# Kernel optimization log

Hardware: AMD Instinct MI355X
Metric: run time of the kernel (lower is better)

Reference implementation:

```python
import jax, jax.numpy as jnp
import numpy as np

B, S, P, I, H, NF, O = 128, 48, 60, 512, 512, 4, 2  # batch, seq_len, pad_size, input_size, hidden, n_filters, output
INITRANGE = 0.1


def setup_inputs() -> dict:
    key = jax.random.key(0)
    ks = jax.random.split(key, 16)
    u = lambda k, shape: jax.random.uniform(k, shape, jnp.float32, -INITRANGE, INITRANGE)
    return {
        "inputs": jax.random.normal(ks[0], (B, S, P, I), jnp.float32),
        # conv: Conv1d(1,1,kernel=input_size,stride=2) == dot product with a length-I vector + scalar bias
        "conv_w": u(ks[1], (I,)),
        "conv_b": u(ks[2], (1,)),
        # bidirectional single-layer GRU params (PyTorch layout: [3H, in], gate order r,z,n)
        "wih_f": u(ks[3], (3 * H, I)), "whh_f": u(ks[4], (3 * H, H)),
        "bih_f": u(ks[5], (3 * H,)), "bhh_f": u(ks[6], (3 * H,)),
        "wih_b": u(ks[7], (3 * H, I)), "whh_b": u(ks[8], (3 * H, H)),
        "bih_b": u(ks[9], (3 * H,)), "bhh_b": u(ks[10], (3 * H,)),
        # conv2: Conv1d(1,n_filters,kernel=hidden*2) == n_filters dot products over the state vector
        "conv2_w": u(ks[11], (NF, 2 * H)),
        "conv2_b": u(ks[12], (NF,)),
        "lin_w": u(ks[13], (O, NF * 2 * H)),
        "lin_b": u(ks[14], (O,)),
        "batch_size": B,
    }


def _gru_dir(x, wih, whh, bih, bhh, reverse):
    # x: [B,S,I]; PyTorch GRU cell math, gate order (r, z, n)
    xp = jnp.einsum("bsi,gi->bsg", x, wih) + bih  # [B,S,3H], input proj hoisted out of scan

    def step(h, xt):
        hp = h @ whh.T + bhh
        xr, xz, xn = jnp.split(xt, 3, axis=-1)
        hr, hz, hn = jnp.split(hp, 3, axis=-1)
        r = jax.nn.sigmoid(xr + hr)
        z = jax.nn.sigmoid(xz + hz)
        n = jnp.tanh(xn + r * hn)
        h_new = (1.0 - z) * n + z * h
        return h_new, h_new

    h0 = jnp.zeros((x.shape[0], whh.shape[1]), x.dtype)
    _, hs = jax.lax.scan(step, h0, jnp.swapaxes(xp, 0, 1), reverse=reverse)
    return jnp.swapaxes(hs, 0, 1)  # [B,S,H], time-major order preserved


def reference(inputs, conv_w, conv_b, wih_f, whh_f, bih_f, bhh_f,
              wih_b, whh_b, bih_b, bhh_b, conv2_w, conv2_b, lin_w, lin_b, batch_size):
    # --- convolutional_layer: per-(visit,code) scalar score, hardtanh(0,1), weighted sum over codes ---
    alpha = jnp.clip(jnp.einsum("bspi,i->bsp", inputs, conv_w) + conv_b[0], 0.0, 1.0)  # [B,S,P]
    emb = jnp.einsum("bsp,bspi->bsi", alpha, inputs)  # [B,S,I]
    # dropout is identity in eval mode
    # --- bidirectional GRU ---
    hf = _gru_dir(emb, wih_f, whh_f, bih_f, bhh_f, reverse=False)
    hb = _gru_dir(emb, wih_b, whh_b, bih_b, bhh_b, reverse=True)
    states = jnp.concatenate([hf, hb], axis=-1)  # [B,S,2H]
    # --- add_beta_attention: n_filters scores per step, softmax over seq, weighted sum of states ---
    logits = jnp.einsum("bsh,fh->bfs", states, conv2_w) + conv2_b[None, :, None]  # [B,F,S]
    beta = jax.nn.softmax(logits, axis=-1)
    context = jnp.einsum("bfs,bsh->bfh", beta, states).reshape(batch_size, -1)  # [B, F*2H]
    out = jax.nn.softmax(context @ lin_w.T + lin_b, axis=-1)  # [B,O]
    return out, alpha, beta
```

## Files before the change

kernel.cpp:

```cpp
#include <hip/hip_runtime.h>

#define B_ 128
#define S_ 48
#define P_ 60
#define I_ 512
#define H_ 512
#define NF_ 4
#define O_ 2

typedef __bf16 bf16x8 __attribute__((ext_vector_type(8)));
typedef float f32x4 __attribute__((ext_vector_type(4)));
typedef unsigned long long u64;

__global__ __launch_bounds__(512, 2) void k_fused(
    const float* __restrict__ inputs, const float* __restrict__ conv_w,
    const float* __restrict__ conv_b,
    const float* __restrict__ whh_f, const float* __restrict__ whh_b,
    const float* __restrict__ wih_f, const float* __restrict__ wih_b,
    const float* __restrict__ bhh_f, const float* __restrict__ bhh_b,
    const float* __restrict__ bih_f, const float* __restrict__ bih_b,
    float* __restrict__ alpha_out,
    unsigned* __restrict__ emb32,
    u64* __restrict__ hbf,
    float* __restrict__ hs,
    unsigned* __restrict__ bar,
    unsigned* __restrict__ percol)
{
  __shared__ __bf16 Ahh[48 * 512];
  __shared__ __bf16 Aih[48 * 512];
  __shared__ float part2[8][512];

  int bid = blockIdx.x;

  if (bid < 128) {
    int dir = bid >> 6;
    int j0  = (bid & 31) * 16;
    int m0  = ((bid >> 5) & 1) * 64;
    int myi = bid & 31;
    int grp = bid >> 5;
    const float* Whh_d = dir ? whh_b : whh_f;
    const float* Wih_d = dir ? wih_b : wih_f;

    for (int it = threadIdx.x; it < 48 * 64; it += 512) {
      int r = it >> 6, c8 = it & 63;
      int grow = (r >> 4) * H_ + j0 + (r & 15);
      int dst = r * 512 + ((c8 ^ (r & 7)) * 8);
      const float* sh = Whh_d + (size_t)grow * I_ + c8 * 8;
      const float* si = Wih_d + (size_t)grow * I_ + c8 * 8;
      float4 a = *(const float4*)(sh), b = *(const float4*)(sh + 4);
      float4 c = *(const float4*)(si), d = *(const float4*)(si + 4);
      bf16x8 oh, oi;
      oh[0]=(__bf16)a.x; oh[1]=(__bf16)a.y; oh[2]=(__bf16)a.z; oh[3]=(__bf16)a.w;
      oh[4]=(__bf16)b.x; oh[5]=(__bf16)b.y; oh[6]=(__bf16)b.z; oh[7]=(__bf16)b.w;
      oi[0]=(__bf16)c.x; oi[1]=(__bf16)c.y; oi[2]=(__bf16)c.z; oi[3]=(__bf16)c.w;
      oi[4]=(__bf16)d.x; oi[5]=(__bf16)d.y; oi[6]=(__bf16)d.z; oi[7]=(__bf16)d.w;
      *(bf16x8*)(Ahh + dst) = oh;
      *(bf16x8*)(Aih + dst) = oi;
    }
    __syncthreads();

    if (threadIdx.x < 256) {
      int wave = threadIdx.x >> 6, lane = threadIdx.x & 63;
      int col = lane & 15, hi = lane >> 4;
      int b = m0 + wave * 16 + col;
      int j = j0 + hi * 4;
      const float* bhh = dir ? bhh_b : bhh_f;
      const float* bih = dir ? bih_b : bih_f;
      float4 bhr = *(const float4*)(bhh + j);
      float4 bhz = *(const float4*)(bhh + H_ + j);
      float4 bhn = *(const float4*)(bhh + 2 * H_ + j);
      float4 bxr = *(const float4*)(bih + j);
      float4 bxz = *(const float4*)(bih + H_ + j);
      float4 bxn = *(const float4*)(bih + 2 * H_ + j);
      float bhhA[3][4] = {{bhr.x,bhr.y,bhr.z,bhr.w},{bhz.x,bhz.y,bhz.z,bhz.w},{bhn.x,bhn.y,bhn.z,bhn.w}};
      float bihA[3][4] = {{bxr.x,bxr.y,bxr.z,bxr.w},{bxz.x,bxz.y,bxz.z,bxz.w},{bxn.x,bxn.y,bxn.z,bxn.w}};
      int rb0 = (0 * 16 + col) * 512, rb1 = (1 * 16 + col) * 512, rb2 = (2 * 16 + col) * 512;
      int csw = col & 7;
      const u64* embB64 = (const u64*)emb32 + (size_t)b * S_ * 128;

      const size_t STEPBUF = (size_t)2 * B_ * (H_ / 4);
      size_t hoff = ((size_t)dir * B_ + b) * (H_ / 4);
      const u64* hd64 = (const u64*)(percol + 48);

      float hprev[4] = {0.f, 0.f, 0.f, 0.f};
      int esent = 0;

      for (int step = 0; step < S_; ++step) {
        int t = dir ? (S_ - 1 - step) : step;

        if (!esent) {
          u64 hd = __hip_atomic_load(hd64, __ATOMIC_RELAXED, __HIP_MEMORY_SCOPE_AGENT);
          if (hd == 0x0000000100000001ull) esent = 1;
          else while (__hip_atomic_load(percol + t, __ATOMIC_RELAXED,
                                        __HIP_MEMORY_SCOPE_AGENT) < 64u) {}
        }

        const u64* erow64 = embB64 + (size_t)t * 128;
        u64 ebu[32];
        #pragma unroll
        for (int kk = 0; kk < 16; ++kk) {
          ebu[2 * kk]     = __hip_atomic_load(erow64 + kk * 8 + hi * 2,
                                              __ATOMIC_RELAXED, __HIP_MEMORY_SCOPE_AGENT);
          ebu[2 * kk + 1] = __hip_atomic_load(erow64 + kk * 8 + hi * 2 + 1,
                                              __ATOMIC_RELAXED, __HIP_MEMORY_SCOPE_AGENT);
        }

        if (step != 0) {
          if (threadIdx.x < 32) {
            const unsigned* pf = bar + (((unsigned)step * 4 + grp) * 32 + threadIdx.x) * 16;
            while (__hip_atomic_load(pf, __ATOMIC_RELAXED, __HIP_MEMORY_SCOPE_AGENT) == 0u) {}
          }
          __syncthreads();
        }

        const u64* hin = hbf + (size_t)step * STEPBUF + hoff;
        u64 hb[32];
        #pragma unroll
        for (int kk = 0; kk < 16; ++kk) {
          hb[2 * kk]     = __hip_atomic_load(hin + kk * 8 + hi * 2, __ATOMIC_RELAXED,
                                             __HIP_MEMORY_SCOPE_AGENT);
          hb[2 * kk + 1] = __hip_atomic_load(hin + kk * 8 + hi * 2 + 1, __ATOMIC_RELAXED,
                                             __HIP_MEMORY_SCOPE_AGENT);
        }

        f32x4 ah0 = {0,0,0,0}, ah1 = {0,0,0,0}, ah2 = {0,0,0,0};
        f32x4 ax0 = {0,0,0,0}, ax1 = {0,0,0,0}, ax2 = {0,0,0,0};
        #pragma unroll
        for (int kk = 0; kk < 16; ++kk) {
          union { u64 u[2]; bf16x8 v; } bu, eu;
          bu.u[0] = hb[2 * kk];
          bu.u[1] = hb[2 * kk + 1];
          eu.u[0] = ebu[2 * kk];
          eu.u[1] = ebu[2 * kk + 1];
          int go = ((kk * 4 + hi) ^ csw) * 8;
          bf16x8 a0 = *(const bf16x8*)(Ahh + rb0 + go);
          bf16x8 a1 = *(const bf16x8*)(Ahh + rb1 + go);
          bf16x8 a2 = *(const bf16x8*)(Ahh + rb2 + go);
          bf16x8 w0 = *(const bf16x8*)(Aih + rb0 + go);
          bf16x8 w1 = *(const bf16x8*)(Aih + rb1 + go);
          bf16x8 w2 = *(const bf16x8*)(Aih + rb2 + go);
          ah0 = __builtin_amdgcn_mfma_f32_16x16x32_bf16(a0, bu.v, ah0, 0, 0, 0);
          ax0 = __builtin_amdgcn_mfma_f32_16x16x32_bf16(w0, eu.v, ax0, 0, 0, 0);
          ah1 = __builtin_amdgcn_mfma_f32_16x16x32_bf16(a1, bu.v, ah1, 0, 0, 0);
          ax1 = __builtin_amdgcn_mfma_f32_16x16x32_bf16(w1, eu.v, ax1, 0, 0, 0);
          ah2 = __builtin_amdgcn_mfma_f32_16x16x32_bf16(a2, bu.v, ah2, 0, 0, 0);
          ax2 = __builtin_amdgcn_mfma_f32_16x16x32_bf16(w2, eu.v, ax2, 0, 0, 0);
        }

        union { u64 u; __bf16 h[4]; } pk;
        #pragma unroll
        for (int r = 0; r < 4; r++) {
          float hr = ah0[r] + bhhA[0][r];
          float hz = ah1[r] + bhhA[1][r];
          float hn = ah2[r] + bhhA[2][r];
          float xr = ax0[r] + bihA[0][r];
          float xz = ax1[r] + bihA[1][r];
          float xn = ax2[r] + bihA[2][r];
          float rg = 1.f / (1.f + __expf(-(xr + hr)));
          float zg = 1.f / (1.f + __expf(-(xz + hz)));
          float ng = tanhf(xn + rg * hn);
          float hnew = (1.f - zg) * ng + zg * hprev[r];
          hprev[r] = hnew;
          pk.h[r] = (__bf16)hnew;
        }

        if (step != S_ - 1) {
          u64* hout = hbf + (size_t)(step + 1) * STEPBUF + hoff;
          __hip_atomic_store(hout + (j0 >> 2) + hi, pk.u, __ATOMIC_RELAXED,
                             __HIP_MEMORY_SCOPE_AGENT);
          __syncthreads();
          if (threadIdx.x == 0)
            __hip_atomic_store(bar + (((unsigned)(step + 1) * 4 + grp) * 32 + myi) * 16,
                               1u, __ATOMIC_RELAXED, __HIP_MEMORY_SCOPE_AGENT);
        }

        float4 hv = {hprev[0], hprev[1], hprev[2], hprev[3]};
        *(float4*)(hs + ((size_t)b * S_ + t) * (2 * H_) + dir * H_ + j) = hv;
      }
    } else {
      for (int step = 0; step < S_; ++step) {
        if (step != 0) __syncthreads();
        if (step != S_ - 1) __syncthreads();
      }
    }
  } else {
    int bid2 = bid - 128;
    int half = bid2 >> 6;
    int blk  = bid2 & 63;
    int bA   = blk * 2;
    int wv   = threadIdx.x >> 6, lane = threadIdx.x & 63;
    int batch = bA + (wv >> 2);
    int wsub  = wv & 3;

    float w[8];
    {
      const float4* c4 = (const float4*)(conv_w + lane * 8);
      float4 a = c4[0], bq = c4[1];
      w[0]=a.x; w[1]=a.y; w[2]=a.z; w[3]=a.w; w[4]=bq.x; w[5]=bq.y; w[6]=bq.z; w[7]=bq.w;
    }
    float cb0 = conv_b[0];

    for (int c = 0; c < 24; ++c) {
      int s = half ? (47 - c) : c;
      const float* xb = inputs + ((size_t)batch * S_ + s) * (P_ * I_);

      float acc[8] = {0,0,0,0,0,0,0,0};
      for (int g = 0; g < 3; ++g) {
        int pbase = wsub + g * 20;
        float xv[5][8];
        float d[5];
        #pragma unroll
        for (int u = 0; u < 5; ++u) {
          const float4* xr = (const float4*)(xb + (size_t)(pbase + 4 * u) * I_ + lane * 8);
          float4 a = xr[0], bq = xr[1];
          xv[u][0]=a.x; xv[u][1]=a.y; xv[u][2]=a.z; xv[u][3]=a.w;
          xv[u][4]=bq.x; xv[u][5]=bq.y; xv[u][6]=bq.z; xv[u][7]=bq.w;
        }
        #pragma unroll
        for (int u = 0; u < 5; ++u) {
          float dd = 0.f;
          #pragma unroll
          for (int jj = 0; jj < 8; jj++) dd += xv[u][jj] * w[jj];
          d[u] = dd;
        }
        #pragma unroll
        for (int off = 32; off >= 1; off >>= 1) {
          #pragma unroll
          for (int u = 0; u < 5; ++u) d[u] += __shfl_xor(d[u], off);
        }
        #pragma unroll
        for (int u = 0; u < 5; ++u) {
          float al = fminf(fmaxf(d[u] + cb0, 0.f), 1.f);
          if (lane == 0) alpha_out[((size_t)batch * S_ + s) * P_ + pbase + 4 * u] = al;
          #pragma unroll
          for (int jj = 0; jj < 8; jj++) acc[jj] += al * xv[u][jj];
        }
      }
      #pragma unroll
      for (int jj = 0; jj < 8; jj++) part2[wv][lane * 8 + jj] = acc[jj];
      __syncthreads();

      {
        int tid = threadIdx.x;
        int bsel = tid >> 8;
        int wbase = bsel * 4;
        int widx = tid & 255;
        int jb = widx * 2;
        float s0 = part2[wbase][jb]   + part2[wbase+1][jb]
                 + part2[wbase+2][jb] + part2[wbase+3][jb];
        float s1 = part2[wbase][jb+1]   + part2[wbase+1][jb+1]
                 + part2[wbase+2][jb+1] + part2[wbase+3][jb+1];
        union { __bf16 h[2]; unsigned u; } up;
        up.h[0] = (__bf16)s0; up.h[1] = (__bf16)s1;
        int bout = bA + bsel;
        __hip_atomic_store(emb32 + ((size_t)bout * S_ + s) * 256 + widx, up.u,
                           __ATOMIC_RELAXED, __HIP_MEMORY_SCOPE_AGENT);
      }
      __syncthreads();
      if (threadIdx.x == 0) {
        unsigned old = __hip_atomic_fetch_add(percol + s, 1u, __ATOMIC_RELAXED,
                                              __HIP_MEMORY_SCOPE_AGENT);
        if (old == 63u && c == 23)
          __hip_atomic_store(percol + 48 + half, 1u, __ATOMIC_RELAXED,
                             __HIP_MEMORY_SCOPE_AGENT);
      }
    }
  }
}

__global__ __launch_bounds__(256) void k_attn(
    const float* __restrict__ hs, const float* __restrict__ c2w,
    const float* __restrict__ c2b, const float* __restrict__ lin_w,
    const float* __restrict__ lin_b, float* __restrict__ out,
    float* __restrict__ beta_out)
{
  int b = blockIdx.x, tid = threadIdx.x;
  const float* st = hs + (size_t)b * S_ * (2 * H_);
  __shared__ float lg[NF_][S_];
  __shared__ float betas[NF_][S_];
  __shared__ float ctx[NF_ * 2 * H_];
  __shared__ float red[2][4];

  if (tid < NF_ * S_) {
    int f = tid / S_, s = tid - f * S_;
    const float4* sv = (const float4*)(st + (size_t)s * (2 * H_));
    const float4* wv = (const float4*)(c2w + (size_t)f * (2 * H_));
    float a = 0.f;
    for (int k = 0; k < 256; k++) {
      float4 x = sv[k], y = wv[k];
      a += x.x * y.x + x.y * y.y + x.z * y.z + x.w * y.w;
    }
    lg[f][s] = a + c2b[f];
  }
  __syncthreads();

  int wv_ = tid >> 6, ln = tid & 63;
  {
    float v = (ln < S_) ? lg[wv_][ln] : -3.4e38f;
    float m = v;
    #pragma unroll
    for (int off = 32; off >= 1; off >>= 1) m = fmaxf(m, __shfl_xor(m, off));
    float e = (ln < S_) ? __expf(v - m) : 0.f;
    float ssum = e;
    #pragma unroll
    for (int off = 32; off >= 1; off >>= 1) ssum += __shfl_xor(ssum, off);
    if (ln < S_) {
      float bta = e / ssum;
      betas[wv_][ln] = bta;
      beta_out[((size_t)b * NF_ + wv_) * S_ + ln] = bta;
    }
  }
  __syncthreads();

  for (int idx = tid; idx < NF_ * 2 * H_; idx += 256) {
    int f = idx >> 10, h = idx & 1023;
    float a = 0.f;
    for (int s = 0; s < S_; s++) a += betas[f][s] * st[(size_t)s * (2 * H_) + h];
    ctx[idx] = a;
  }
  __syncthreads();

  float p0 = 0.f, p1 = 0.f;
  for (int idx = tid; idx < NF_ * 2 * H_; idx += 256) {
    float c = ctx[idx];
    p0 += c * lin_w[idx];
    p1 += c * lin_w[NF_ * 2 * H_ + idx];
  }
  #pragma unroll
  for (int off = 32; off >= 1; off >>= 1) {
    p0 += __shfl_xor(p0, off);
    p1 += __shfl_xor(p1, off);
  }
  if (ln == 0) { red[0][wv_] = p0; red[1][wv_] = p1; }
  __syncthreads();
  if (tid == 0) {
    float l0 = red[0][0] + red[0][1] + red[0][2] + red[0][3] + lin_b[0];
    float l1 = red[1][0] + red[1][1] + red[1][2] + red[1][3] + lin_b[1];
    float m = fmaxf(l0, l1);
    float e0 = __expf(l0 - m), e1 = __expf(l1 - m);
    float s = e0 + e1;
    out[(size_t)b * O_ + 0] = e0 / s;
    out[(size_t)b * O_ + 1] = e1 / s;
  }
}

extern "C" void kernel_launch(void* const* d_in, const int* in_sizes, int n_in,
                              void* d_out, int out_size, void* d_ws, size_t ws_size,
                              hipStream_t stream) {
  const float* inputs = (const float*)d_in[0];
  const float* conv_w = (const float*)d_in[1];
  const float* conv_b = (const float*)d_in[2];
  const float* wih_f  = (const float*)d_in[3];
  const float* whh_f  = (const float*)d_in[4];
  const float* bih_f  = (const float*)d_in[5];
  const float* bhh_f  = (const float*)d_in[6];
  const float* wih_b  = (const float*)d_in[7];
  const float* whh_b  = (const float*)d_in[8];
  const float* bih_b  = (const float*)d_in[9];
  const float* bhh_b  = (const float*)d_in[10];
  const float* c2w    = (const float*)d_in[11];
  const float* c2b    = (const float*)d_in[12];
  const float* lin_w  = (const float*)d_in[13];
  const float* lin_b  = (const float*)d_in[14];

  float* out   = (float*)d_out;
  float* alpha = out + B_ * O_;
  float* beta  = alpha + (size_t)B_ * S_ * P_;

  char* ws = (char*)d_ws;
  unsigned* emb32 = (unsigned*)ws;
  float*  hs      = (float*)(ws + 6291456);
  unsigned* bar   = (unsigned*)(ws + 31457280);
  unsigned* percol= (unsigned*)(ws + 31850496);
  u64*    hbf     = (u64*)(ws + 31858688);

  hipMemsetAsync((void*)bar, 0, 401408 + 262144, stream);

  {
    float* alpha_arg = alpha;
    void* args[] = {(void*)&inputs, (void*)&conv_w, (void*)&conv_b,
                    (void*)&whh_f, (void*)&whh_b, (void*)&wih_f, (void*)&wih_b,
                    (void*)&bhh_f, (void*)&bhh_b, (void*)&bih_f, (void*)&bih_b,
                    (void*)&alpha_arg, (void*)&emb32, (void*)&hbf, (void*)&hs,
                    (void*)&bar, (void*)&percol};
    hipLaunchCooperativeKernel((void*)k_fused, dim3(256), dim3(512), args, 0, stream);
  }

  k_attn<<<B_, 256, 0, stream>>>(hs, c2w, c2b, lin_w, lin_b, out, beta);
}
```

Baseline: 574.3 us.

## Use full 8-wave GRU blocks and three producer teams for embedding

Halves the number of recurrent GRU blocks by having each block process all 128 batch rows with all 8 waves, instead of leaving half its waves idle. The freed blocks become a third producer team, and timesteps are interleaved from both ends across teams. Completion signalling moves to a single counter of finished timesteps. The aim is to speed up the memory-bound embedding phase and cut barrier participants, at the cost of more MFMA work per block per serial step.

```diff
diff --git a/kernel.cpp b/kernel.cpp
--- a/kernel.cpp
+++ b/kernel.cpp
@@ -32,12 +32,11 @@
 
   int bid = blockIdx.x;
 
-  if (bid < 128) {
-    int dir = bid >> 6;
+  if (bid < 64) {
+    int dir = bid >> 5;
     int j0  = (bid & 31) * 16;
-    int m0  = ((bid >> 5) & 1) * 64;
     int myi = bid & 31;
-    int grp = bid >> 5;
+    int grp = dir;
     const float* Whh_d = dir ? whh_b : whh_f;
     const float* Wih_d = dir ? wih_b : wih_f;
 
@@ -59,134 +58,126 @@
     }
     __syncthreads();
 
-    if (threadIdx.x < 256) {
-      int wave = threadIdx.x >> 6, lane = threadIdx.x & 63;
-      int col = lane & 15, hi = lane >> 4;
-      int b = m0 + wave * 16 + col;
-      int j = j0 + hi * 4;
-      const float* bhh = dir ? bhh_b : bhh_f;
-      const float* bih = dir ? bih_b : bih_f;
-      float4 bhr = *(const float4*)(bhh + j);
-      float4 bhz = *(const float4*)(bhh + H_ + j);
-      float4 bhn = *(const float4*)(bhh + 2 * H_ + j);
-      float4 bxr = *(const float4*)(bih + j);
-      float4 bxz = *(const float4*)(bih + H_ + j);
-      float4 bxn = *(const float4*)(bih + 2 * H_ + j);
-      float bhhA[3][4] = {{bhr.x,bhr.y,bhr.z,bhr.w},{bhz.x,bhz.y,bhz.z,bhz.w},{bhn.x,bhn.y,bhn.z,bhn.w}};
-      float bihA[3][4] = {{bxr.x,bxr.y,bxr.z,bxr.w},{bxz.x,bxz.y,bxz.z,bxz.w},{bxn.x,bxn.y,bxn.z,bxn.w}};
-      int rb0 = (0 * 16 + col) * 512, rb1 = (1 * 16 + col) * 512, rb2 = (2 * 16 + col) * 512;
-      int csw = col & 7;
-      const u64* embB64 = (const u64*)emb32 + (size_t)b * S_ * 128;
-
-      const size_t STEPBUF = (size_t)2 * B_ * (H_ / 4);
-      size_t hoff = ((size_t)dir * B_ + b) * (H_ / 4);
-      const u64* hd64 = (const u64*)(percol + 48);
-
-      float hprev[4] = {0.f, 0.f, 0.f, 0.f};
-      int esent = 0;
-
-      for (int step = 0; step < S_; ++step) {
-        int t = dir ? (S_ - 1 - step) : step;
-
-        if (!esent) {
-          u64 hd = __hip_atomic_load(hd64, __ATOMIC_RELAXED, __HIP_MEMORY_SCOPE_AGENT);
-          if (hd == 0x0000000100000001ull) esent = 1;
-          else while (__hip_atomic_load(percol + t, __ATOMIC_RELAXED,
-                                        __HIP_MEMORY_SCOPE_AGENT) < 64u) {}
-        }
-
-        const u64* erow64 = embB64 + (size_t)t * 128;
-        u64 ebu[32];
-        #pragma unroll
-        for (int kk = 0; kk < 16; ++kk) {
-          ebu[2 * kk]     = __hip_atomic_load(erow64 + kk * 8 + hi * 2,
-                                              __ATOMIC_RELAXED, __HIP_MEMORY_SCOPE_AGENT);
-          ebu[2 * kk + 1] = __hip_atomic_load(erow64 + kk * 8 + hi * 2 + 1,
-                                              __ATOMIC_RELAXED, __HIP_MEMORY_SCOPE_AGENT);
-        }
-
-        if (step != 0) {
-          if (threadIdx.x < 32) {
-            const unsigned* pf = bar + (((unsigned)step * 4 + grp) * 32 + threadIdx.x) * 16;
-            while (__hip_atomic_load(pf, __ATOMIC_RELAXED, __HIP_MEMORY_SCOPE_AGENT) == 0u) {}
-          }
-          __syncthreads();
-        }
-
-        const u64* hin = hbf + (size_t)step * STEPBUF + hoff;
-        u64 hb[32];
-        #pragma unroll
-        for (int kk = 0; kk < 16; ++kk) {
-          hb[2 * kk]     = __hip_atomic_load(hin + kk * 8 + hi * 2, __ATOMIC_RELAXED,
-                                             __HIP_MEMORY_SCOPE_AGENT);
-          hb[2 * kk + 1] = __hip_atomic_load(hin + kk * 8 + hi * 2 + 1, __ATOMIC_RELAXED,
-                                             __HIP_MEMORY_SCOPE_AGENT);
-        }
-
-        f32x4 ah0 = {0,0,0,0}, ah1 = {0,0,0,0}, ah2 = {0,0,0,0};
-        f32x4 ax0 = {0,0,0,0}, ax1 = {0,0,0,0}, ax2 = {0,0,0,0};
-        #pragma unroll
-        for (int kk = 0; kk < 16; ++kk) {
-          union { u64 u[2]; bf16x8 v; } bu, eu;
-          bu.u[0] = hb[2 * kk];
-          bu.u[1] = hb[2 * kk + 1];
-          eu.u[0] = ebu[2 * kk];
-          eu.u[1] = ebu[2 * kk + 1];
-          int go = ((kk * 4 + hi) ^ csw) * 8;
-          bf16x8 a0 = *(const bf16x8*)(Ahh + rb0 + go);
-          bf16x8 a1 = *(const bf16x8*)(Ahh + rb1 + go);
-          bf16x8 a2 = *(const bf16x8*)(Ahh + rb2 + go);
-          bf16x8 w0 = *(const bf16x8*)(Aih + rb0 + go);
-          bf16x8 w1 = *(const bf16x8*)(Aih + rb1 + go);
-          bf16x8 w2 = *(const bf16x8*)(Aih + rb2 + go);
-          ah0 = __builtin_amdgcn_mfma_f32_16x16x32_bf16(a0, bu.v, ah0, 0, 0, 0);
-          ax0 = __builtin_amdgcn_mfma_f32_16x16x32_bf16(w0, eu.v, ax0, 0, 0, 0);
-          ah1 = __builtin_amdgcn_mfma_f32_16x16x32_bf16(a1, bu.v, ah1, 0, 0, 0);
-          ax1 = __builtin_amdgcn_mfma_f32_16x16x32_bf16(w1, eu.v, ax1, 0, 0, 0);
-          ah2 = __builtin_amdgcn_mfma_f32_16x16x32_bf16(a2, bu.v, ah2, 0, 0, 0);
-          ax2 = __builtin_amdgcn_mfma_f32_16x16x32_bf16(w2, eu.v, ax2, 0, 0, 0);
-        }
-
-        union { u64 u; __bf16 h[4]; } pk;
-        #pragma unroll
-        for (int r = 0; r < 4; r++) {
-          float hr = ah0[r] + bhhA[0][r];
-          float hz = ah1[r] + bhhA[1][r];
-          float hn = ah2[r] + bhhA[2][r];
-          float xr = ax0[r] + bihA[0][r];
-          float xz = ax1[r] + bihA[1][r];
-          float xn = ax2[r] + bihA[2][r];
-          float rg = 1.f / (1.f + __expf(-(xr + hr)));
-          float zg = 1.f / (1.f + __expf(-(xz + hz)));
-          float ng = tanhf(xn + rg * hn);
-          float hnew = (1.f - zg) * ng + zg * hprev[r];
-          hprev[r] = hnew;
-          pk.h[r] = (__bf16)hnew;
-        }
-
-        if (step != S_ - 1) {
-          u64* hout = hbf + (size_t)(step + 1) * STEPBUF + hoff;
-          __hip_atomic_store(hout + (j0 >> 2) + hi, pk.u, __ATOMIC_RELAXED,
-                             __HIP_MEMORY_SCOPE_AGENT);
-          __syncthreads();
-          if (threadIdx.x == 0)
-            __hip_atomic_store(bar + (((unsigned)(step + 1) * 4 + grp) * 32 + myi) * 16,
-                               1u, __ATOMIC_RELAXED, __HIP_MEMORY_SCOPE_AGENT);
-        }
-
-        float4 hv = {hprev[0], hprev[1], hprev[2], hprev[3]};
-        *(float4*)(hs + ((size_t)b * S_ + t) * (2 * H_) + dir * H_ + j) = hv;
-      }
-    } else {
-      for (int step = 0; step < S_; ++step) {
-        if (step != 0) __syncthreads();
-        if (step != S_ - 1) __syncthreads();
-      }
+    int wave = threadIdx.x >> 6, lane = threadIdx.x & 63;
+    int col = lane & 15, hi = lane >> 4;
+    int b = wave * 16 + col;
+    int j = j0 + hi * 4;
+    const float* bhh = dir ? bhh_b : bhh_f;
+    const float* bih = dir ? bih_b : bih_f;
+    float4 bhr = *(const float4*)(bhh + j);
+    float4 bhz = *(const float4*)(bhh + H_ + j);
+    float4 bhn = *(const float4*)(bhh + 2 * H_ + j);
+    float4 bxr = *(const float4*)(bih + j);
+    float4 bxz = *(const float4*)(bih + H_ + j);
+    float4 bxn = *(const float4*)(bih + 2 * H_ + j);
+    float bhhA[3][4] = {{bhr.x,bhr.y,bhr.z,bhr.w},{bhz.x,bhz.y,bhz.z,bhz.w},{bhn.x,bhn.y,bhn.z,bhn.w}};
+    float bihA[3][4] = {{bxr.x,bxr.y,bxr.z,bxr.w},{bxz.x,bxz.y,bxz.z,bxz.w},{bxn.x,bxn.y,bxn.z,bxn.w}};
+    int rb0 = (0 * 16 + col) * 512, rb1 = (1 * 16 + col) * 512, rb2 = (2 * 16 + col) * 512;
+    int csw = col & 7;
+    const u64* embB64 = (const u64*)emb32 + (size_t)b * S_ * 128;
+
+    const size_t STEPBUF = (size_t)2 * B_ * (H_ / 4);
+    size_t hoff = ((size_t)dir * B_ + b) * (H_ / 4);
+
+    float hprev[4] = {0.f, 0.f, 0.f, 0.f};
+    int esent = 0;
+
+    for (int step = 0; step < S_; ++step) {
+      int t = dir ? (S_ - 1 - step) : step;
+
+      if (!esent) {
+        if (__hip_atomic_load(percol + 56, __ATOMIC_RELAXED,
+                              __HIP_MEMORY_SCOPE_AGENT) == 48u) esent = 1;
+        else while (__hip_atomic_load(percol + t, __ATOMIC_RELAXED,
+                                      __HIP_MEMORY_SCOPE_AGENT) < 64u) {}
+      }
+
+      const u64* erow64 = embB64 + (size_t)t * 128;
+      u64 ebu[32];
+      #pragma unroll
+      for (int kk = 0; kk < 16; ++kk) {
+        ebu[2 * kk]     = __hip_atomic_load(erow64 + kk * 8 + hi * 2,
+                                            __ATOMIC_RELAXED, __HIP_MEMORY_SCOPE_AGENT);
+        ebu[2 * kk + 1] = __hip_atomic_load(erow64 + kk * 8 + hi * 2 + 1,
+                                            __ATOMIC_RELAXED, __HIP_MEMORY_SCOPE_AGENT);
+      }
+
+      if (step != 0) {
+        if (threadIdx.x < 32) {
+          const unsigned* pf = bar + (((unsigned)step * 2 + grp) * 32 + threadIdx.x) * 16;
+          while (__hip_atomic_load(pf, __ATOMIC_RELAXED, __HIP_MEMORY_SCOPE_AGENT) == 0u) {}
+        }
+        __syncthreads();
+      }
+
+      const u64* hin = hbf + (size_t)step * STEPBUF + hoff;
+      u64 hb[32];
+      #pragma unroll
+      for (int kk = 0; kk < 16; ++kk) {
+        hb[2 * kk]     = __hip_atomic_load(hin + kk * 8 + hi * 2, __ATOMIC_RELAXED,
+                                           __HIP_MEMORY_SCOPE_AGENT);
+        hb[2 * kk + 1] = __hip_atomic_load(hin + kk * 8 + hi * 2 + 1, __ATOMIC_RELAXED,
+                                           __HIP_MEMORY_SCOPE_AGENT);
+      }
+
+      f32x4 ah0 = {0,0,0,0}, ah1 = {0,0,0,0}, ah2 = {0,0,0,0};
+      f32x4 ax0 = {0,0,0,0}, ax1 = {0,0,0,0}, ax2 = {0,0,0,0};
+      #pragma unroll
+      for (int kk = 0; kk < 16; ++kk) {
+        union { u64 u[2]; bf16x8 v; } bu, eu;
+        bu.u[0] = hb[2 * kk];
+        bu.u[1] = hb[2 * kk + 1];
+        eu.u[0] = ebu[2 * kk];
+        eu.u[1] = ebu[2 * kk + 1];
+        int go = ((kk * 4 + hi) ^ csw) * 8;
+        bf16x8 a0 = *(const bf16x8*)(Ahh + rb0 + go);
+        bf16x8 a1 = *(const bf16x8*)(Ahh + rb1 + go);
+        bf16x8 a2 = *(const bf16x8*)(Ahh + rb2 + go);
+        bf16x8 w0 = *(const bf16x8*)(Aih + rb0 + go);
+        bf16x8 w1 = *(const bf16x8*)(Aih + rb1 + go);
+        bf16x8 w2 = *(const bf16x8*)(Aih + rb2 + go);
+        ah0 = __builtin_amdgcn_mfma_f32_16x16x32_bf16(a0, bu.v, ah0, 0, 0, 0);
+        ax0 = __builtin_amdgcn_mfma_f32_16x16x32_bf16(w0, eu.v, ax0, 0, 0, 0);
+        ah1 = __builtin_amdgcn_mfma_f32_16x16x32_bf16(a1, bu.v, ah1, 0, 0, 0);
+        ax1 = __builtin_amdgcn_mfma_f32_16x16x32_bf16(w1, eu.v, ax1, 0, 0, 0);
+        ah2 = __builtin_amdgcn_mfma_f32_16x16x32_bf16(a2, bu.v, ah2, 0, 0, 0);
+        ax2 = __builtin_amdgcn_mfma_f32_16x16x32_bf16(w2, eu.v, ax2, 0, 0, 0);
+      }
+
+      union { u64 u; __bf16 h[4]; } pk;
+      #pragma unroll
+      for (int r = 0; r < 4; r++) {
+        float hr = ah0[r] + bhhA[0][r];
+        float hz = ah1[r] + bhhA[1][r];
+        float hn = ah2[r] + bhhA[2][r];
+        float xr = ax0[r] + bihA[0][r];
+        float xz = ax1[r] + bihA[1][r];
+        float xn = ax2[r] + bihA[2][r];
+        float rg = 1.f / (1.f + __expf(-(xr + hr)));
+        float zg = 1.f / (1.f + __expf(-(xz + hz)));
+        float ng = tanhf(xn + rg * hn);
+        float hnew = (1.f - zg) * ng + zg * hprev[r];
+        hprev[r] = hnew;
+        pk.h[r] = (__bf16)hnew;
+      }
+
+      if (step != S_ - 1) {
+        u64* hout = hbf + (size_t)(step + 1) * STEPBUF + hoff;
+        __hip_atomic_store(hout + (j0 >> 2) + hi, pk.u, __ATOMIC_RELAXED,
+                           __HIP_MEMORY_SCOPE_AGENT);
+        __syncthreads();
+        if (threadIdx.x == 0)
+          __hip_atomic_store(bar + (((unsigned)(step + 1) * 2 + grp) * 32 + myi) * 16,
+                             1u, __ATOMIC_RELAXED, __HIP_MEMORY_SCOPE_AGENT);
+      }
+
+      float4 hv = {hprev[0], hprev[1], hprev[2], hprev[3]};
+      *(float4*)(hs + ((size_t)b * S_ + t) * (2 * H_) + dir * H_ + j) = hv;
     }
   } else {
-    int bid2 = bid - 128;
-    int half = bid2 >> 6;
-    int blk  = bid2 & 63;
+    int pid  = bid - 64;
+    int team = pid >> 6;
+    int blk  = pid & 63;
     int bA   = blk * 2;
     int wv   = threadIdx.x >> 6, lane = threadIdx.x & 63;
     int batch = bA + (wv >> 2);
@@ -200,8 +191,9 @@
     }
     float cb0 = conv_b[0];
 
-    for (int c = 0; c < 24; ++c) {
-      int s = half ? (47 - c) : c;
+    for (int k = 0; k < 16; ++k) {
+      int q = team + 3 * k;
+      int s = (q & 1) ? (47 - (q >> 1)) : (q >> 1);
       const float* xb = inputs + ((size_t)batch * S_ + s) * (P_ * I_);
 
       float acc[8] = {0,0,0,0,0,0,0,0};
@@ -260,9 +252,9 @@
       if (threadIdx.x == 0) {
         unsigned old = __hip_atomic_fetch_add(percol + s, 1u, __ATOMIC_RELAXED,
                                               __HIP_MEMORY_SCOPE_AGENT);
-        if (old == 63u && c == 23)
-          __hip_atomic_store(percol + 48 + half, 1u, __ATOMIC_RELAXED,
-                             __HIP_MEMORY_SCOPE_AGENT);
+        if (old == 63u)
+          __hip_atomic_fetch_add(percol + 56, 1u, __ATOMIC_RELAXED,
+                                 __HIP_MEMORY_SCOPE_AGENT);
       }
     }
   }
```

Measured after the change: 892.6 us. 55.4% more time.
